# Kernel tuning notes

Hardware: AMD Instinct MI355X
Metric: run time of the kernel (lower is better)

## Reference

```python
import jax, jax.numpy as jnp
import numpy as np

B, P, D = 16, 512, 1024   # batch, num wordpieces, bert_dim (roberta-large)
W, T, E = 400, 32, 64     # num words, num triggers (spans), num entities (spans)
H = 600                   # hidden_num of role_idn_ffn


def _make_idxs(rng, b, m, n, max_len):
    # [start, end) intervals with 0 <= start < end <= n, sorted starts per row
    starts = np.sort(rng.integers(0, n - 1, size=(b, m)), axis=1)
    ends = np.minimum(starts + rng.integers(1, max_len + 1, size=(b, m)), n)
    ends = np.maximum(ends, starts + 1)
    return np.stack([starts, ends], axis=-1).astype(np.int32)


def setup_inputs() -> dict:
    key = jax.random.key(0)
    k1, k2, k3 = jax.random.split(key, 3)
    rng = np.random.default_rng(0)
    return {
        "piece_reprs": jax.random.normal(k1, (B, P, D), dtype=jnp.float32),
        "word_idxs": jnp.asarray(_make_idxs(rng, B, W, P, 4)),
        "trigger_idxs": jnp.asarray(_make_idxs(rng, B, T, W, 8)),
        "entity_idxs": jnp.asarray(_make_idxs(rng, B, E, W, 12)),
        "W0": jax.random.normal(k2, (4 * D, H), dtype=jnp.float32) * 0.02,
        "b0": jnp.zeros((H,), dtype=jnp.float32),
        "W1": jax.random.normal(k3, (H, 2), dtype=jnp.float32) * 0.02,
        "b1": jnp.zeros((2,), dtype=jnp.float32),
    }


def _segment_mean(x, idxs):
    """Mean of x[b, start:end] per interval. x: [B,N,Dm], idxs: [B,M,2] -> [B,M,Dm].
    Vectorized replacement of the nested-loop slice+mean via inclusive prefix sums."""
    cs = jnp.concatenate([jnp.zeros_like(x[:, :1]), jnp.cumsum(x, axis=1)], axis=1)  # [B,N+1,Dm]
    s = jnp.take_along_axis(cs, idxs[:, :, 0:1], axis=1)  # [B,M,Dm]
    e = jnp.take_along_axis(cs, idxs[:, :, 1:2], axis=1)  # [B,M,Dm]
    lens = (idxs[:, :, 1] - idxs[:, :, 0]).astype(x.dtype)[:, :, None]
    return (e - s) / lens


def reference(piece_reprs, word_idxs, trigger_idxs, entity_idxs, W0, b0, W1, b1):
    # encode(): wordpiece -> word averaging (compute_word_reps_avg)
    word_reprs = _segment_mean(piece_reprs, word_idxs)          # [B, W, D]
    # scores(): span mean pooling (compute_span_reprs)
    trig = _segment_mean(word_reprs, trigger_idxs)              # [B, T, D]
    ent = _segment_mean(word_reprs, entity_idxs)                # [B, E, D]
    b, t, d = trig.shape
    e = ent.shape[1]
    # compute_binary_reprs: all (trigger, entity) pairs, trigger index varies slowly
    t_rep = jnp.broadcast_to(trig[:, :, None, :], (b, t, e, d)).reshape(b, t * e, d)
    e_rep = jnp.broadcast_to(ent[:, None, :, :], (b, t, e, d)).reshape(b, t * e, d)
    role = jnp.concatenate([t_rep, e_rep, t_rep * e_rep, jnp.abs(t_rep - e_rep)], axis=-1)  # [B,T*E,4D]
    # role_idn_ffn: Linears([4D, H, 2]) with relu between layers (dropout=0 at eval)
    h = jax.nn.relu(role @ W0 + b0)
    return h @ W1 + b1                                          # [B, T*E, 2]
```

## Files before the change

kernel.cpp:

```cpp
#include <hip/hip_runtime.h>
#include <cstddef>
#include <cstdint>

typedef float f32x4 __attribute__((ext_vector_type(4)));
typedef __bf16 bf16x8 __attribute__((ext_vector_type(8)));
typedef __bf16 bf16x4 __attribute__((ext_vector_type(4)));

constexpr int NB = 16;
constexpr int NP = 512;
constexpr int ND = 1024;
constexpr int NW = 400;
constexpr int NT = 32;
constexpr int NE = 64;
constexpr int NH = 600;
constexpr int IMGP = 128 * 64;
constexpr int IMGQ = 320 * 64;

__device__ inline bf16x8 pack8(float a0, float a1, float a2, float a3,
                               float a4, float a5, float a6, float a7) {
    bf16x8 v;
    v[0] = (__bf16)a0; v[1] = (__bf16)a1; v[2] = (__bf16)a2; v[3] = (__bf16)a3;
    v[4] = (__bf16)a4; v[5] = (__bf16)a5; v[6] = (__bf16)a6; v[7] = (__bf16)a7;
    return v;
}

__device__ inline void dma16(const void* g, void* l) {
    __builtin_amdgcn_global_load_lds(
        (const __attribute__((address_space(1))) uint32_t*)g,
        (__attribute__((address_space(3))) uint32_t*)l, 16, 0, 0);
}

__global__ __launch_bounds__(256) void word_mean_kernel(
    const float* __restrict__ piece, const int* __restrict__ widx,
    float* __restrict__ word) {
    int bw = blockIdx.x;
    int b = bw / NW;
    int s = widx[bw * 2], e = widx[bw * 2 + 1];
    int col = threadIdx.x * 4;
    const float* base = piece + (size_t)b * NP * ND + col;
    float4 acc = make_float4(0.f, 0.f, 0.f, 0.f);
    for (int r = s; r < e; ++r) {
        float4 v = *(const float4*)(base + (size_t)r * ND);
        acc.x += v.x; acc.y += v.y; acc.z += v.z; acc.w += v.w;
    }
    float inv = 1.0f / (float)(e - s);
    acc.x *= inv; acc.y *= inv; acc.z *= inv; acc.w *= inv;
    *(float4*)(word + (size_t)bw * ND + col) = acc;
}

__global__ __launch_bounds__(256) void span_mean_kernel(
    const float* __restrict__ word, const int* __restrict__ tidx,
    const int* __restrict__ eidx, float* __restrict__ trig,
    float* __restrict__ ent) {
    int id = blockIdx.x;
    const int* idx;
    float* out;
    int b;
    if (id < NB * NT) {
        b = id / NT; idx = tidx + id * 2; out = trig + (size_t)id * ND;
    } else {
        int id2 = id - NB * NT;
        b = id2 / NE; idx = eidx + id2 * 2; out = ent + (size_t)id2 * ND;
    }
    int s = idx[0], e = idx[1];
    int col = threadIdx.x * 4;
    const float* base = word + (size_t)b * NW * ND + col;
    float4 acc = make_float4(0.f, 0.f, 0.f, 0.f);
    for (int r = s; r < e; ++r) {
        float4 v = *(const float4*)(base + (size_t)r * ND);
        acc.x += v.x; acc.y += v.y; acc.z += v.z; acc.w += v.w;
    }
    float inv = 1.0f / (float)(e - s);
    acc.x *= inv; acc.y *= inv; acc.z *= inv; acc.w *= inv;
    *(float4*)(out + col) = acc;
}

__global__ __launch_bounds__(256) void w0_swizzle_kernel(
    const float* __restrict__ W0, __bf16* __restrict__ W0pre) {
    __shared__ float T[64][132];
    int kb = blockIdx.x, nc = blockIdx.y;
    int t = threadIdx.x;
    {
        int kl = t >> 2;
        int n0 = (t & 3) * 32;
        int kg = kb * 64 + kl;
        const float* src = W0 + (size_t)kg * NH + nc * 128 + n0;
#pragma unroll
        for (int g = 0; g < 8; ++g) {
            int n = nc * 128 + n0 + g * 4;
            float4 v = (n < NH) ? *(const float4*)(src + g * 4)
                                : make_float4(0.f, 0.f, 0.f, 0.f);
            *(float4*)&T[kl][n0 + g * 4] = v;
        }
    }
    __syncthreads();
#pragma unroll
    for (int s = 0; s < 4; ++s) {
        int idx = t * 4 + s;
        int row = idx >> 3, c = idx & 7;
        bf16x8 v = pack8(T[c * 8 + 0][row], T[c * 8 + 1][row],
                         T[c * 8 + 2][row], T[c * 8 + 3][row],
                         T[c * 8 + 4][row], T[c * 8 + 5][row],
                         T[c * 8 + 6][row], T[c * 8 + 7][row]);
        __bf16* img = W0pre + ((size_t)nc * 32 + kb) * IMGP;
        *(bf16x8*)&img[row * 64 + ((c ^ (row & 7)) << 3)] = v;
    }
}

__global__ __launch_bounds__(256) void w0_pair_kernel(
    const float* __restrict__ W0, __bf16* __restrict__ W0pair) {
    __shared__ float T[64][84];
    int it = blockIdx.x, nc = blockIdx.y, zz = blockIdx.z;
    int tid = threadIdx.x;
    {
        int kidx = tid >> 2, npart = tid & 3;
        int korig = 2048 + (kidx >> 5) * 1024 + it * 32 + (kidx & 31);
        const float* src = W0 + (size_t)korig * NH;
        int nbase = nc * 320 + zz * 80 + npart * 20;
#pragma unroll
        for (int g = 0; g < 5; ++g) {
            int n = nbase + g * 4;
            float4 v = (n < NH) ? *(const float4*)(src + n)
                                : make_float4(0.f, 0.f, 0.f, 0.f);
            *(float4*)&T[kidx][npart * 20 + g * 4] = v;
        }
    }
    __syncthreads();
    __bf16* img = W0pair + ((size_t)nc * 32 + it) * IMGQ + (size_t)zz * 80 * 64;
#pragma unroll
    for (int s = 0; s < 3; ++s) {
        int idx = s * 256 + tid;
        if (idx < 640) {
            int r = idx >> 3, c = idx & 7;
            bf16x8 v = pack8(T[c * 8 + 0][r], T[c * 8 + 1][r],
                             T[c * 8 + 2][r], T[c * 8 + 3][r],
                             T[c * 8 + 4][r], T[c * 8 + 5][r],
                             T[c * 8 + 6][r], T[c * 8 + 7][r]);
            int slot = (c + (r & 7)) & 7;
            *(bf16x8*)&img[r * 64 + slot * 8] = v;
        }
    }
}

__global__ __launch_bounds__(64) void pre_mfma_kernel(
    const float* __restrict__ trig, const float* __restrict__ ent,
    const __bf16* __restrict__ W0pre, float* __restrict__ pre_t,
    float* __restrict__ pre_e) {
    __shared__ __bf16 As[64 * 64];
    __shared__ __bf16 Bs[64 * 64];
    int mt8 = blockIdx.x, ntile = blockIdx.y;
    const float* A;
    float* C;
    int kbofs, mbase;
    if (mt8 < 8) { A = trig; C = pre_t; kbofs = 0;  mbase = mt8 * 64; }
    else         { A = ent;  C = pre_e; kbofs = 16; mbase = (mt8 - 8) * 64; }
    int lane = threadIdx.x;
    int q = lane >> 4, l15 = lane & 15, sa = l15 & 7;
    int nc = ntile >> 1, half = ntile & 1;
    const __bf16* imgbase =
        W0pre + ((size_t)nc * 32 + kbofs) * IMGP + half * 4096;
    f32x4 acc[4][4] = {};

    for (int it = 0; it < 16; ++it) {
        __syncthreads();
        const __bf16* img = imgbase + (size_t)it * IMGP;
#pragma unroll
        for (int i = 0; i < 8; ++i)
            dma16(img + i * 512 + lane * 8, (__bf16*)Bs + i * 512);
#pragma unroll
        for (int s = 0; s < 8; ++s) {
            int L = s * 64 + lane;
            int r = L >> 3, c = L & 7;
            const float* ar = A + (size_t)(mbase + r) * ND + it * 64 + c * 8;
            float4 a0 = *(const float4*)ar, a1 = *(const float4*)(ar + 4);
            *(bf16x8*)&As[r * 64 + ((c ^ (r & 7)) << 3)] =
                pack8(a0.x, a0.y, a0.z, a0.w, a1.x, a1.y, a1.z, a1.w);
        }
        __syncthreads();
#pragma unroll
        for (int ks = 0; ks < 2; ++ks) {
            int coff = ((q ^ sa) ^ (ks << 2)) << 3;
            bf16x8 af[4];
#pragma unroll
            for (int mt = 0; mt < 4; ++mt)
                af[mt] = *(const bf16x8*)&As[(16 * mt + l15) * 64 + coff];
#pragma unroll
            for (int nt = 0; nt < 4; ++nt) {
                bf16x8 bf = *(const bf16x8*)&Bs[(16 * nt + l15) * 64 + coff];
#pragma unroll
                for (int mt = 0; mt < 4; ++mt)
                    acc[mt][nt] = __builtin_amdgcn_mfma_f32_16x16x32_bf16(
                        af[mt], bf, acc[mt][nt], 0, 0, 0);
            }
        }
    }
#pragma unroll
    for (int mt = 0; mt < 4; ++mt)
#pragma unroll
        for (int r = 0; r < 4; ++r) {
            float* crow = C + (size_t)(mbase + 16 * mt + 4 * q + r) * NH;
#pragma unroll
            for (int nt = 0; nt < 4; ++nt) {
                int n = ntile * 64 + 16 * nt + l15;
                if (n < NH) crow[n] = acc[mt][nt][r];
            }
        }
}

__global__ __launch_bounds__(256, 2) void pair_mfma_kernel(
    const float* __restrict__ trig, const float* __restrict__ ent,
    const __bf16* __restrict__ W0pair, const float* __restrict__ b0,
    const float* __restrict__ pre_t, const float* __restrict__ pre_e,
    const float* __restrict__ W1, const float* __restrict__ b1,
    float* __restrict__ out) {
    __shared__ __bf16 Xs[128 * 64];
    __shared__ __bf16 Bs[320 * 64];
    __shared__ __bf16 Ts[2 * 1024];
    int b = blockIdx.x, tp = blockIdx.y, nc = blockIdx.z;
    int tid = threadIdx.x;
    int lane = tid & 63, w = tid >> 6, rw = w & 1, cw = w >> 1;
    int q = lane >> 4, l15 = lane & 15, s7 = l15 & 7;
    int xrow = tid >> 1, xh = tid & 1;
    int xr7 = xrow & 7;
    const float* t0row = trig + (size_t)(b * NT + tp * 2 + 0) * ND;
    const float* t1row = trig + (size_t)(b * NT + tp * 2 + 1) * ND;
    const float* erow = ent + (size_t)(b * NE + (xrow & 63)) * ND;
    const __bf16* imgbase = W0pair + (size_t)nc * 32 * IMGQ;
    f32x4 acc[4][10] = {};
    float4 ef4[4];

    auto dma_b = [&](int it) {
        const __bf16* img = imgbase + (size_t)it * IMGQ + w * 5120;
        __bf16* lds = (__bf16*)Bs + w * 5120;
#pragma unroll
        for (int i = 0; i < 10; ++i)
            dma16(img + i * 512 + lane * 8, lds + i * 512);
    };
    auto load_e = [&](int it) {
        const float* er = erow + it * 32 + xh * 16;
#pragma unroll
        for (int i = 0; i < 4; ++i) ef4[i] = *(const float4*)(er + i * 4);
    };
    auto write_x = [&](int it) {
        const __bf16* tsrc = &Ts[(xrow >> 6) * 1024 + it * 32 + xh * 16];
        bf16x8 tlo = *(const bf16x8*)tsrc;
        bf16x8 thi = *(const bf16x8*)(tsrc + 8);
        float tf[16], ef[16];
#pragma unroll
        for (int j = 0; j < 8; ++j) { tf[j] = (float)tlo[j]; tf[8 + j] = (float)thi[j]; }
        ef[0] = ef4[0].x; ef[1] = ef4[0].y; ef[2] = ef4[0].z; ef[3] = ef4[0].w;
        ef[4] = ef4[1].x; ef[5] = ef4[1].y; ef[6] = ef4[1].z; ef[7] = ef4[1].w;
        ef[8] = ef4[2].x; ef[9] = ef4[2].y; ef[10] = ef4[2].z; ef[11] = ef4[2].w;
        ef[12] = ef4[3].x; ef[13] = ef4[3].y; ef[14] = ef4[3].z; ef[15] = ef4[3].w;
        int base = xrow * 64;
        int sp0 = ((2 * xh + 0 + xr7) & 7) * 8;
        int sp1 = ((2 * xh + 1 + xr7) & 7) * 8;
        int sd0 = ((2 * xh + 4 + xr7) & 7) * 8;
        int sd1 = ((2 * xh + 5 + xr7) & 7) * 8;
        *(bf16x8*)&Xs[base + sp0] = pack8(
            tf[0] * ef[0], tf[1] * ef[1], tf[2] * ef[2], tf[3] * ef[3],
            tf[4] * ef[4], tf[5] * ef[5], tf[6] * ef[6], tf[7] * ef[7]);
        *(bf16x8*)&Xs[base + sp1] = pack8(
            tf[8] * ef[8], tf[9] * ef[9], tf[10] * ef[10], tf[11] * ef[11],
            tf[12] * ef[12], tf[13] * ef[13], tf[14] * ef[14], tf[15] * ef[15]);
        *(bf16x8*)&Xs[base + sd0] = pack8(
            fabsf(tf[0] - ef[0]), fabsf(tf[1] - ef[1]),
            fabsf(tf[2] - ef[2]), fabsf(tf[3] - ef[3]),
            fabsf(tf[4] - ef[4]), fabsf(tf[5] - ef[5]),
            fabsf(tf[6] - ef[6]), fabsf(tf[7] - ef[7]));
        *(bf16x8*)&Xs[base + sd1] = pack8(
            fabsf(tf[8] - ef[8]), fabsf(tf[9] - ef[9]),
            fabsf(tf[10] - ef[10]), fabsf(tf[11] - ef[11]),
            fabsf(tf[12] - ef[12]), fabsf(tf[13] - ef[13]),
            fabsf(tf[14] - ef[14]), fabsf(tf[15] - ef[15]));
    };
    auto mfma_tile = [&]() {
#pragma unroll
        for (int ks = 0; ks < 2; ++ks) {
            int slot = ((4 * ks + q + s7) & 7) * 8;
            bf16x8 af[4];
#pragma unroll
            for (int mt = 0; mt < 4; ++mt)
                af[mt] = *(const bf16x8*)&Xs[(64 * rw + 16 * mt + l15) * 64 + slot];
#pragma unroll
            for (int nt = 0; nt < 10; ++nt) {
                bf16x8 bfv =
                    *(const bf16x8*)&Bs[(160 * cw + 16 * nt + l15) * 64 + slot];
#pragma unroll
                for (int mt = 0; mt < 4; ++mt)
                    acc[mt][nt] = __builtin_amdgcn_mfma_f32_16x16x32_bf16(
                        af[mt], bfv, acc[mt][nt], 0, 0, 0);
            }
        }
    };

    {
        int k0 = tid * 4;
        float4 va = *(const float4*)(t0row + k0);
        float4 vb = *(const float4*)(t1row + k0);
        bf16x4 pa, pb;
        pa[0] = (__bf16)va.x; pa[1] = (__bf16)va.y;
        pa[2] = (__bf16)va.z; pa[3] = (__bf16)va.w;
        pb[0] = (__bf16)vb.x; pb[1] = (__bf16)vb.y;
        pb[2] = (__bf16)vb.z; pb[3] = (__bf16)vb.w;
        *(bf16x4*)&Ts[k0] = pa;
        *(bf16x4*)&Ts[1024 + k0] = pb;
    }
    dma_b(0);
    load_e(0);
    __syncthreads();
    write_x(0);
    __syncthreads();

    for (int it = 0; it < 32; ++it) {
        if (it < 31) load_e(it + 1);
        mfma_tile();
        __syncthreads();
        if (it < 31) {
            dma_b(it + 1);
            write_x(it + 1);
            __syncthreads();
        }
    }

    int tglob = b * NT + tp * 2 + rw;
    const float* preT = pre_t + (size_t)tglob * NH;
    float w10[10], w11[10], b0v[10], ptv[10];
    int nbase = nc * 320 + 160 * cw + l15;
#pragma unroll
    for (int nt = 0; nt < 10; ++nt) {
        int n = nbase + 16 * nt;
        bool v = n < NH;
        w10[nt] = v ? W1[2 * n] : 0.f;
        w11[nt] = v ? W1[2 * n + 1] : 0.f;
        b0v[nt] = v ? b0[n] : 0.f;
        ptv[nt] = v ? preT[n] : 0.f;
    }
    float b10 = b1[0], b11 = b1[1];
    bool lead = (l15 == 0);
    bool addb = (nc == 0) && (cw == 0);
#pragma unroll
    for (int mt = 0; mt < 4; ++mt) {
#pragma unroll
        for (int r = 0; r < 4; ++r) {
            int e = 16 * mt + 4 * q + r;
            const float* preE = pre_e + (size_t)(b * NE + e) * NH;
            float s0 = 0.f, s1 = 0.f;
#pragma unroll
            for (int nt = 0; nt < 10; ++nt) {
                int n = nbase + 16 * nt;
                float pe = (n < NH) ? preE[n] : 0.f;
                float h = acc[mt][nt][r] + ptv[nt] + pe + b0v[nt];
                h = fmaxf(h, 0.f);
                s0 += h * w10[nt];
                s1 += h * w11[nt];
            }
#pragma unroll
            for (int m = 8; m >= 1; m >>= 1) {
                s0 += __shfl_xor(s0, m);
                s1 += __shfl_xor(s1, m);
            }
            if (lead) {
                if (addb) { s0 += b10; s1 += b11; }
                float* o = out + ((size_t)(tglob * NE + e)) * 2;
                atomicAdd(o, s0);
                atomicAdd(o + 1, s1);
            }
        }
    }
}

extern "C" void kernel_launch(void* const* d_in, const int* in_sizes, int n_in,
                              void* d_out, int out_size, void* d_ws,
                              size_t ws_size, hipStream_t stream) {
    const float* piece = (const float*)d_in[0];
    const int* widx = (const int*)d_in[1];
    const int* tidx = (const int*)d_in[2];
    const int* eidx = (const int*)d_in[3];
    const float* W0 = (const float*)d_in[4];
    const float* b0 = (const float*)d_in[5];
    const float* W1 = (const float*)d_in[6];
    const float* b1 = (const float*)d_in[7];
    float* out = (float*)d_out;

    float* ws = (float*)d_ws;
    float* word = ws;
    float* trig = word + (size_t)NB * NW * ND;
    float* ent = trig + (size_t)NB * NT * ND;
    float* pre_t = ent + (size_t)NB * NE * ND;
    float* pre_e = pre_t + (size_t)NB * NT * NH;
    __bf16* W0pre = (__bf16*)word;
    __bf16* W0pair = W0pre + (size_t)5 * 32 * IMGP;

    hipMemsetAsync(d_out, 0, (size_t)out_size * sizeof(float), stream);

    word_mean_kernel<<<NB * NW, 256, 0, stream>>>(piece, widx, word);
    span_mean_kernel<<<NB * (NT + NE), 256, 0, stream>>>(word, tidx, eidx, trig, ent);
    w0_swizzle_kernel<<<dim3(32, 5), 256, 0, stream>>>(W0, W0pre);
    w0_pair_kernel<<<dim3(32, 2, 4), 256, 0, stream>>>(W0, W0pair);
    pre_mfma_kernel<<<dim3(24, 10), 64, 0, stream>>>(trig, ent, W0pre, pre_t, pre_e);
    pair_mfma_kernel<<<dim3(16, 16, 2), 256, 0, stream>>>(
        trig, ent, W0pair, b0, pre_t, pre_e, W1, b1, out);
}
```

Baseline: 226.3 us.

## Double-buffer pair GEMM with K=32 stages and enlarge pre-GEMM tiles

The pair MFMA kernel now uses two LDS buffers with a K-step of 32 (64 iterations). The next weight DMA and X-tile construction overlap the current MFMAs, leaving one barrier per iteration instead of two. The weight image layout and swizzle are rebuilt for 32-wide rows to match. Separately, pre_mfma now uses 256-thread blocks with 128x128 tiles instead of 64-thread 64x64 blocks. The shorter K step costs more loop iterations and barriers, and LDS use per block changes slightly.

```diff
diff --git a/kernel.cpp b/kernel.cpp
--- a/kernel.cpp
+++ b/kernel.cpp
@@ -4,7 +4,6 @@
 
 typedef float f32x4 __attribute__((ext_vector_type(4)));
 typedef __bf16 bf16x8 __attribute__((ext_vector_type(8)));
-typedef __bf16 bf16x4 __attribute__((ext_vector_type(4)));
 
 constexpr int NB = 16;
 constexpr int NP = 512;
@@ -14,7 +13,7 @@
 constexpr int NE = 64;
 constexpr int NH = 600;
 constexpr int IMGP = 128 * 64;
-constexpr int IMGQ = 320 * 64;
+constexpr int IMGQ = 320 * 32;
 
 __device__ inline bf16x8 pack8(float a0, float a1, float a2, float a3,
                                float a4, float a5, float a6, float a7) {
@@ -109,72 +108,73 @@
 
 __global__ __launch_bounds__(256) void w0_pair_kernel(
     const float* __restrict__ W0, __bf16* __restrict__ W0pair) {
-    __shared__ float T[64][84];
+    __shared__ float T[32][84];
     int it = blockIdx.x, nc = blockIdx.y, zz = blockIdx.z;
     int tid = threadIdx.x;
     {
-        int kidx = tid >> 2, npart = tid & 3;
-        int korig = 2048 + (kidx >> 5) * 1024 + it * 32 + (kidx & 31);
+        int kidx = tid >> 3, part = tid & 7;
+        int korig = (kidx < 16) ? (2048 + it * 16 + kidx)
+                                : (3072 + it * 16 + (kidx - 16));
         const float* src = W0 + (size_t)korig * NH;
-        int nbase = nc * 320 + zz * 80 + npart * 20;
-#pragma unroll
-        for (int g = 0; g < 5; ++g) {
-            int n = nbase + g * 4;
-            float4 v = (n < NH) ? *(const float4*)(src + n)
-                                : make_float4(0.f, 0.f, 0.f, 0.f);
-            *(float4*)&T[kidx][npart * 20 + g * 4] = v;
+#pragma unroll
+        for (int g = 0; g < 10; ++g) {
+            int n = nc * 320 + zz * 80 + part * 10 + g;
+            T[kidx][part * 10 + g] = (n < NH) ? src[n] : 0.0f;
         }
     }
     __syncthreads();
-    __bf16* img = W0pair + ((size_t)nc * 32 + it) * IMGQ + (size_t)zz * 80 * 64;
-#pragma unroll
-    for (int s = 0; s < 3; ++s) {
+    __bf16* img = W0pair + ((size_t)nc * 64 + it) * IMGQ;
+#pragma unroll
+    for (int s = 0; s < 2; ++s) {
         int idx = s * 256 + tid;
-        if (idx < 640) {
-            int r = idx >> 3, c = idx & 7;
-            bf16x8 v = pack8(T[c * 8 + 0][r], T[c * 8 + 1][r],
-                             T[c * 8 + 2][r], T[c * 8 + 3][r],
-                             T[c * 8 + 4][r], T[c * 8 + 5][r],
-                             T[c * 8 + 6][r], T[c * 8 + 7][r]);
-            int slot = (c + (r & 7)) & 7;
-            *(bf16x8*)&img[r * 64 + slot * 8] = v;
-        }
-    }
-}
-
-__global__ __launch_bounds__(64) void pre_mfma_kernel(
+        if (idx < 320) {
+            int rloc = idx >> 2, c = idx & 3;
+            bf16x8 v = pack8(T[c * 8 + 0][rloc], T[c * 8 + 1][rloc],
+                             T[c * 8 + 2][rloc], T[c * 8 + 3][rloc],
+                             T[c * 8 + 4][rloc], T[c * 8 + 5][rloc],
+                             T[c * 8 + 6][rloc], T[c * 8 + 7][rloc]);
+            int rg = zz * 80 + rloc;
+            int slot = ((rg >> 1) + c) & 3;
+            *(bf16x8*)&img[rg * 32 + slot * 8] = v;
+        }
+    }
+}
+
+__global__ __launch_bounds__(256) void pre_mfma_kernel(
     const float* __restrict__ trig, const float* __restrict__ ent,
     const __bf16* __restrict__ W0pre, float* __restrict__ pre_t,
     float* __restrict__ pre_e) {
-    __shared__ __bf16 As[64 * 64];
-    __shared__ __bf16 Bs[64 * 64];
-    int mt8 = blockIdx.x, ntile = blockIdx.y;
+    __shared__ __bf16 As[128 * 64];
+    __shared__ __bf16 Bs[128 * 64];
+    int mb = blockIdx.x, nc = blockIdx.y;
     const float* A;
     float* C;
     int kbofs, mbase;
-    if (mt8 < 8) { A = trig; C = pre_t; kbofs = 0;  mbase = mt8 * 64; }
-    else         { A = ent;  C = pre_e; kbofs = 16; mbase = (mt8 - 8) * 64; }
-    int lane = threadIdx.x;
+    if (mb < 4) { A = trig; C = pre_t; kbofs = 0;  mbase = mb * 128; }
+    else        { A = ent;  C = pre_e; kbofs = 16; mbase = (mb - 4) * 128; }
+    int tid = threadIdx.x;
+    int lane = tid & 63, w = tid >> 6, rw = w & 1, cw = w >> 1;
     int q = lane >> 4, l15 = lane & 15, sa = l15 & 7;
-    int nc = ntile >> 1, half = ntile & 1;
-    const __bf16* imgbase =
-        W0pre + ((size_t)nc * 32 + kbofs) * IMGP + half * 4096;
+    int ar = tid >> 1, ah = tid & 1;
+    const __bf16* imgbase = W0pre + ((size_t)nc * 32 + kbofs) * IMGP;
     f32x4 acc[4][4] = {};
 
     for (int it = 0; it < 16; ++it) {
         __syncthreads();
-        const __bf16* img = imgbase + (size_t)it * IMGP;
-#pragma unroll
-        for (int i = 0; i < 8; ++i)
-            dma16(img + i * 512 + lane * 8, (__bf16*)Bs + i * 512);
-#pragma unroll
-        for (int s = 0; s < 8; ++s) {
-            int L = s * 64 + lane;
-            int r = L >> 3, c = L & 7;
-            const float* ar = A + (size_t)(mbase + r) * ND + it * 64 + c * 8;
-            float4 a0 = *(const float4*)ar, a1 = *(const float4*)(ar + 4);
-            *(bf16x8*)&As[r * 64 + ((c ^ (r & 7)) << 3)] =
-                pack8(a0.x, a0.y, a0.z, a0.w, a1.x, a1.y, a1.z, a1.w);
+        const __bf16* img = imgbase + (size_t)it * IMGP + w * 2048;
+#pragma unroll
+        for (int i = 0; i < 4; ++i)
+            dma16(img + i * 512 + lane * 8, (__bf16*)Bs + w * 2048 + i * 512);
+        {
+            const float* src = A + (size_t)(mbase + ar) * ND + it * 64 + ah * 32;
+#pragma unroll
+            for (int i = 0; i < 4; ++i) {
+                float4 a0 = *(const float4*)(src + i * 8);
+                float4 a1 = *(const float4*)(src + i * 8 + 4);
+                int c = ah * 4 + i;
+                *(bf16x8*)&As[ar * 64 + ((c ^ (ar & 7)) << 3)] =
+                    pack8(a0.x, a0.y, a0.z, a0.w, a1.x, a1.y, a1.z, a1.w);
+            }
         }
         __syncthreads();
 #pragma unroll
@@ -183,10 +183,10 @@
             bf16x8 af[4];
 #pragma unroll
             for (int mt = 0; mt < 4; ++mt)
-                af[mt] = *(const bf16x8*)&As[(16 * mt + l15) * 64 + coff];
+                af[mt] = *(const bf16x8*)&As[(64 * rw + 16 * mt + l15) * 64 + coff];
 #pragma unroll
             for (int nt = 0; nt < 4; ++nt) {
-                bf16x8 bf = *(const bf16x8*)&Bs[(16 * nt + l15) * 64 + coff];
+                bf16x8 bf = *(const bf16x8*)&Bs[(64 * cw + 16 * nt + l15) * 64 + coff];
 #pragma unroll
                 for (int mt = 0; mt < 4; ++mt)
                     acc[mt][nt] = __builtin_amdgcn_mfma_f32_16x16x32_bf16(
@@ -198,10 +198,11 @@
     for (int mt = 0; mt < 4; ++mt)
 #pragma unroll
         for (int r = 0; r < 4; ++r) {
-            float* crow = C + (size_t)(mbase + 16 * mt + 4 * q + r) * NH;
+            float* crow =
+                C + (size_t)(mbase + 64 * rw + 16 * mt + 4 * q + r) * NH;
 #pragma unroll
             for (int nt = 0; nt < 4; ++nt) {
-                int n = ntile * 64 + 16 * nt + l15;
+                int n = nc * 128 + 64 * cw + 16 * nt + l15;
                 if (n < NH) crow[n] = acc[mt][nt][r];
             }
         }
@@ -213,114 +214,94 @@
     const float* __restrict__ pre_t, const float* __restrict__ pre_e,
     const float* __restrict__ W1, const float* __restrict__ b1,
     float* __restrict__ out) {
-    __shared__ __bf16 Xs[128 * 64];
-    __shared__ __bf16 Bs[320 * 64];
-    __shared__ __bf16 Ts[2 * 1024];
+    __shared__ __bf16 Xs[2][128 * 32];
+    __shared__ __bf16 Bs[2][320 * 32];
+    __shared__ __bf16 Ts[2048];
     int b = blockIdx.x, tp = blockIdx.y, nc = blockIdx.z;
     int tid = threadIdx.x;
     int lane = tid & 63, w = tid >> 6, rw = w & 1, cw = w >> 1;
-    int q = lane >> 4, l15 = lane & 15, s7 = l15 & 7;
-    int xrow = tid >> 1, xh = tid & 1;
-    int xr7 = xrow & 7;
-    const float* t0row = trig + (size_t)(b * NT + tp * 2 + 0) * ND;
-    const float* t1row = trig + (size_t)(b * NT + tp * 2 + 1) * ND;
-    const float* erow = ent + (size_t)(b * NE + (xrow & 63)) * ND;
-    const __bf16* imgbase = W0pair + (size_t)nc * 32 * IMGQ;
+    int q = lane >> 4, l15 = lane & 15;
+    int xr = tid >> 1, xh = tid & 1;
+    const float* t0row = trig + (size_t)(b * NT + tp * 2) * ND;
+    const float* erow = ent + (size_t)(b * NE + (xr & 63)) * ND;
+    const __bf16* imgbase = W0pair + (size_t)nc * 64 * IMGQ;
     f32x4 acc[4][10] = {};
-    float4 ef4[4];
-
-    auto dma_b = [&](int it) {
-        const __bf16* img = imgbase + (size_t)it * IMGQ + w * 5120;
-        __bf16* lds = (__bf16*)Bs + w * 5120;
-#pragma unroll
-        for (int i = 0; i < 10; ++i)
+    float4 ef4[2];
+
+    auto dma_b = [&](int it, int buf) {
+        const __bf16* img = imgbase + (size_t)it * IMGQ + w * 2560;
+        __bf16* lds = &Bs[buf][w * 2560];
+#pragma unroll
+        for (int i = 0; i < 5; ++i)
             dma16(img + i * 512 + lane * 8, lds + i * 512);
     };
     auto load_e = [&](int it) {
-        const float* er = erow + it * 32 + xh * 16;
-#pragma unroll
-        for (int i = 0; i < 4; ++i) ef4[i] = *(const float4*)(er + i * 4);
+        const float* er = erow + it * 16 + xh * 8;
+        ef4[0] = *(const float4*)er;
+        ef4[1] = *(const float4*)(er + 4);
     };
-    auto write_x = [&](int it) {
-        const __bf16* tsrc = &Ts[(xrow >> 6) * 1024 + it * 32 + xh * 16];
-        bf16x8 tlo = *(const bf16x8*)tsrc;
-        bf16x8 thi = *(const bf16x8*)(tsrc + 8);
-        float tf[16], ef[16];
-#pragma unroll
-        for (int j = 0; j < 8; ++j) { tf[j] = (float)tlo[j]; tf[8 + j] = (float)thi[j]; }
+    auto write_x = [&](int it, int buf) {
+        bf16x8 tv = *(const bf16x8*)&Ts[(xr >> 6) * 1024 + it * 16 + xh * 8];
+        float tf[8], ef[8];
+#pragma unroll
+        for (int j = 0; j < 8; ++j) tf[j] = (float)tv[j];
         ef[0] = ef4[0].x; ef[1] = ef4[0].y; ef[2] = ef4[0].z; ef[3] = ef4[0].w;
         ef[4] = ef4[1].x; ef[5] = ef4[1].y; ef[6] = ef4[1].z; ef[7] = ef4[1].w;
-        ef[8] = ef4[2].x; ef[9] = ef4[2].y; ef[10] = ef4[2].z; ef[11] = ef4[2].w;
-        ef[12] = ef4[3].x; ef[13] = ef4[3].y; ef[14] = ef4[3].z; ef[15] = ef4[3].w;
-        int base = xrow * 64;
-        int sp0 = ((2 * xh + 0 + xr7) & 7) * 8;
-        int sp1 = ((2 * xh + 1 + xr7) & 7) * 8;
-        int sd0 = ((2 * xh + 4 + xr7) & 7) * 8;
-        int sd1 = ((2 * xh + 5 + xr7) & 7) * 8;
-        *(bf16x8*)&Xs[base + sp0] = pack8(
+        int sp = (((xr >> 1) + xh) & 3) * 8;
+        int sd = (((xr >> 1) + 2 + xh) & 3) * 8;
+        __bf16* xb = &Xs[buf][xr * 32];
+        *(bf16x8*)(xb + sp) = pack8(
             tf[0] * ef[0], tf[1] * ef[1], tf[2] * ef[2], tf[3] * ef[3],
             tf[4] * ef[4], tf[5] * ef[5], tf[6] * ef[6], tf[7] * ef[7]);
-        *(bf16x8*)&Xs[base + sp1] = pack8(
-            tf[8] * ef[8], tf[9] * ef[9], tf[10] * ef[10], tf[11] * ef[11],
-            tf[12] * ef[12], tf[13] * ef[13], tf[14] * ef[14], tf[15] * ef[15]);
-        *(bf16x8*)&Xs[base + sd0] = pack8(
+        *(bf16x8*)(xb + sd) = pack8(
             fabsf(tf[0] - ef[0]), fabsf(tf[1] - ef[1]),
             fabsf(tf[2] - ef[2]), fabsf(tf[3] - ef[3]),
             fabsf(tf[4] - ef[4]), fabsf(tf[5] - ef[5]),
             fabsf(tf[6] - ef[6]), fabsf(tf[7] - ef[7]));
-        *(bf16x8*)&Xs[base + sd1] = pack8(
-            fabsf(tf[8] - ef[8]), fabsf(tf[9] - ef[9]),
-            fabsf(tf[10] - ef[10]), fabsf(tf[11] - ef[11]),
-            fabsf(tf[12] - ef[12]), fabsf(tf[13] - ef[13]),
-            fabsf(tf[14] - ef[14]), fabsf(tf[15] - ef[15]));
     };
-    auto mfma_tile = [&]() {
-#pragma unroll
-        for (int ks = 0; ks < 2; ++ks) {
-            int slot = ((4 * ks + q + s7) & 7) * 8;
-            bf16x8 af[4];
+    auto mfma_tile = [&](int buf) {
+        const __bf16* X = Xs[buf];
+        const __bf16* Bb = Bs[buf];
+        bf16x8 af[4];
+#pragma unroll
+        for (int mt = 0; mt < 4; ++mt) {
+            int r = 64 * rw + 16 * mt + l15;
+            af[mt] = *(const bf16x8*)&X[r * 32 + (((r >> 1) + q) & 3) * 8];
+        }
+#pragma unroll
+        for (int nt = 0; nt < 10; ++nt) {
+            int r = 160 * cw + 16 * nt + l15;
+            bf16x8 bv = *(const bf16x8*)&Bb[r * 32 + (((r >> 1) + q) & 3) * 8];
 #pragma unroll
             for (int mt = 0; mt < 4; ++mt)
-                af[mt] = *(const bf16x8*)&Xs[(64 * rw + 16 * mt + l15) * 64 + slot];
-#pragma unroll
-            for (int nt = 0; nt < 10; ++nt) {
-                bf16x8 bfv =
-                    *(const bf16x8*)&Bs[(160 * cw + 16 * nt + l15) * 64 + slot];
-#pragma unroll
-                for (int mt = 0; mt < 4; ++mt)
-                    acc[mt][nt] = __builtin_amdgcn_mfma_f32_16x16x32_bf16(
-                        af[mt], bfv, acc[mt][nt], 0, 0, 0);
-            }
+                acc[mt][nt] = __builtin_amdgcn_mfma_f32_16x16x32_bf16(
+                    af[mt], bv, acc[mt][nt], 0, 0, 0);
         }
     };
 
     {
-        int k0 = tid * 4;
-        float4 va = *(const float4*)(t0row + k0);
-        float4 vb = *(const float4*)(t1row + k0);
-        bf16x4 pa, pb;
-        pa[0] = (__bf16)va.x; pa[1] = (__bf16)va.y;
-        pa[2] = (__bf16)va.z; pa[3] = (__bf16)va.w;
-        pb[0] = (__bf16)vb.x; pb[1] = (__bf16)vb.y;
-        pb[2] = (__bf16)vb.z; pb[3] = (__bf16)vb.w;
-        *(bf16x4*)&Ts[k0] = pa;
-        *(bf16x4*)&Ts[1024 + k0] = pb;
-    }
-    dma_b(0);
+        int k0 = (tid & 127) * 8;
+        const float* src = t0row + (tid >> 7) * ND + k0;
+        float4 va = *(const float4*)src;
+        float4 vb = *(const float4*)(src + 4);
+        *(bf16x8*)&Ts[tid * 8] =
+            pack8(va.x, va.y, va.z, va.w, vb.x, vb.y, vb.z, vb.w);
+    }
+    dma_b(0, 0);
     load_e(0);
     __syncthreads();
-    write_x(0);
+    write_x(0, 0);
     __syncthreads();
 
-    for (int it = 0; it < 32; ++it) {
-        if (it < 31) load_e(it + 1);
-        mfma_tile();
+    for (int it = 0; it < 64; ++it) {
+        int cur = it & 1, nxt = cur ^ 1;
+        if (it < 63) {
+            load_e(it + 1);
+            dma_b(it + 1, nxt);
+        }
+        mfma_tile(cur);
+        if (it < 63) write_x(it + 1, nxt);
         __syncthreads();
-        if (it < 31) {
-            dma_b(it + 1);
-            write_x(it + 1);
-            __syncthreads();
-        }
     }
 
     int tglob = b * NT + tp * 2 + rw;
@@ -397,8 +378,8 @@
     word_mean_kernel<<<NB * NW, 256, 0, stream>>>(piece, widx, word);
     span_mean_kernel<<<NB * (NT + NE), 256, 0, stream>>>(word, tidx, eidx, trig, ent);
     w0_swizzle_kernel<<<dim3(32, 5), 256, 0, stream>>>(W0, W0pre);
-    w0_pair_kernel<<<dim3(32, 2, 4), 256, 0, stream>>>(W0, W0pair);
-    pre_mfma_kernel<<<dim3(24, 10), 64, 0, stream>>>(trig, ent, W0pre, pre_t, pre_e);
+    w0_pair_kernel<<<dim3(64, 2, 4), 256, 0, stream>>>(W0, W0pair);
+    pre_mfma_kernel<<<dim3(12, 5), 256, 0, stream>>>(trig, ent, W0pre, pre_t, pre_e);
     pair_mfma_kernel<<<dim3(16, 16, 2), 256, 0, stream>>>(
         trig, ent, W0pair, b0, pre_t, pre_e, W1, b1, out);
 }
```

New measurement: 251.0 us. +10.9%, slower.
